# Optimization experiments

Measured on AMD Instinct MI355X. Metric: run time of the kernel, lower is better.

Reference implementation:

```python
import jax, jax.numpy as jnp
import numpy as np

N = 100000
E = 640000
D = 128      # node_dim == edge_dim
H = 256      # conv MLP hidden dim
EPS = 1e-5


def _ln(x, g, b):
    mu = jnp.mean(x, axis=-1, keepdims=True)
    var = jnp.var(x, axis=-1, keepdims=True)
    return (x - mu) * jax.lax.rsqrt(var + EPS) * g + b


def _conv_mlp(x, W1, b1, g1, be1, W2, b2, g2, be2):
    h = _ln(x @ W1 + b1, g1, be1)          # (N, H)
    h = jax.nn.relu(h)
    return _ln(h @ W2 + b2, g2, be2)        # (N, D)


def setup_inputs() -> dict:
    key = jax.random.key(0)
    ks = jax.random.split(key, 6)
    s1 = 1.0 / np.sqrt(D)
    s2 = 1.0 / np.sqrt(H)
    return {
        "x": jax.random.normal(ks[0], (N, D), dtype=jnp.float32),
        "edge_index": jax.random.randint(ks[1], (2, E), 0, N, dtype=jnp.int32),
        "edge_attr": jax.random.normal(ks[2], (E, D), dtype=jnp.float32),
        "W1": jax.random.uniform(ks[3], (D, H), jnp.float32, -s1, s1),
        "b1": jnp.zeros((H,), jnp.float32),
        "g1": jnp.ones((H,), jnp.float32),
        "be1": jnp.zeros((H,), jnp.float32),
        "W2": jax.random.uniform(ks[4], (H, D), jnp.float32, -s2, s2),
        "b2": jnp.zeros((D,), jnp.float32),
        "g2": jnp.ones((D,), jnp.float32),
        "be2": jnp.zeros((D,), jnp.float32),
        "g_out": jnp.ones((D,), jnp.float32),
        "b_out": jnp.zeros((D,), jnp.float32),
    }


def reference(x, edge_index, edge_attr, W1, b1, g1, be1, W2, b2, g2, be2, g_out, b_out):
    # Conv(h[w]) for all nodes once, then gather per edge (vectorized form of
    # the per-node/per-neighbor loops in the torch module).
    conv = _conv_mlp(x, W1, b1, g1, be1, W2, b2, g2, be2)   # (N, D)
    src, dst = edge_index[0], edge_index[1]
    msgs = conv[dst] * edge_attr                            # (E, D): Conv(h[w]) * e[v,w]
    agg = jax.ops.segment_sum(msgs, src, num_segments=N)    # scatter-add into v
    return _ln(agg + x, g_out, b_out)
```

## Files before the change

### kernel.cpp

```cpp
#include <hip/hip_runtime.h>

constexpr int D = 128;
constexpr int H = 256;
constexpr float EPS = 1e-5f;

typedef __attribute__((ext_vector_type(8))) __bf16  bf16x8;
typedef __attribute__((ext_vector_type(4))) float   f32x4;

static __device__ __forceinline__ unsigned short f2bfu(float f) {
    unsigned u = __float_as_uint(f);
    return (unsigned short)((u + 0x7FFFu + ((u >> 16) & 1u)) >> 16);
}
static __device__ __forceinline__ float bf2f(unsigned short u) {
    return __uint_as_float((unsigned)u << 16);
}

static __device__ __forceinline__ f32x4 mfma16x16x32(bf16x8 a, bf16x8 b, f32x4 c) {
    return __builtin_amdgcn_mfma_f32_16x16x32_bf16(a, b, c, 0, 0, 0);
}

static __device__ __forceinline__ void pack_w_elem(
    const float* __restrict__ W, unsigned short* __restrict__ Wp, int K, int Ncols, int e)
{
    int i  = e & 7;
    int l  = (e >> 3) & 63;
    int jt = e >> 9;
    int nt = K >> 5;
    int j  = jt / nt;
    int t  = jt - j * nt;
    int k  = 32 * t + ((l >> 4) << 3) + i;
    int c  = 16 * j + (l & 15);
    Wp[e] = f2bfu(W[(size_t)k * Ncols + c]);
}

__global__ __launch_bounds__(256) void prep_kernel(
    const float* __restrict__ W1, unsigned short* __restrict__ W1p,
    const float* __restrict__ W2, unsigned short* __restrict__ W2p,
    int* __restrict__ counts, int N)
{
    int b = blockIdx.x;
    if (b < 128) {
        pack_w_elem(W1, W1p, D, H, b * 256 + threadIdx.x);
    } else if (b < 256) {
        pack_w_elem(W2, W2p, H, D, (b - 128) * 256 + threadIdx.x);
    } else {
        int i = (b - 256) * 256 + threadIdx.x;
        if (i < N) counts[i] = 0;
    }
}

static __device__ void conv_body(
    unsigned short* __restrict__ Hs,
    const float* __restrict__ x,
    const unsigned short* __restrict__ W1p, const float* __restrict__ b1,
    const float* __restrict__ g1, const float* __restrict__ be1,
    const unsigned short* __restrict__ W2p, const float* __restrict__ b2,
    const float* __restrict__ g2, const float* __restrict__ be2,
    unsigned short* __restrict__ convb, int N, int cblk)
{
    const int wv   = threadIdx.x >> 6;
    const int lane = threadIdx.x & 63;
    const int rrow = lane & 15;
    const int kgrp = lane >> 4;
    const int r0   = cblk * 64 + wv * 16;

    int arow = r0 + rrow; if (arow >= N) arow = N - 1;
    const float* xr = x + (size_t)arow * D + kgrp * 8;
    bf16x8 A1[4];
    #pragma unroll
    for (int t = 0; t < 4; ++t) {
        float4 fa = *(const float4*)(xr + t * 32);
        float4 fb = *(const float4*)(xr + t * 32 + 4);
        bf16x8 a;
        a[0] = (__bf16)fa.x; a[1] = (__bf16)fa.y; a[2] = (__bf16)fa.z; a[3] = (__bf16)fa.w;
        a[4] = (__bf16)fb.x; a[5] = (__bf16)fb.y; a[6] = (__bf16)fb.z; a[7] = (__bf16)fb.w;
        A1[t] = a;
    }

    f32x4 acc[16];
    #pragma unroll
    for (int j = 0; j < 16; ++j) acc[j] = (f32x4){0.f, 0.f, 0.f, 0.f};
    const bf16x8* w1f = (const bf16x8*)W1p;
    #pragma unroll
    for (int j = 0; j < 16; ++j) {
        #pragma unroll
        for (int t = 0; t < 4; ++t) {
            bf16x8 B = w1f[(j * 4 + t) * 64 + lane];
            acc[j] = mfma16x16x32(A1[t], B, acc[j]);
        }
    }

    float b1r[16], g1r[16], be1r[16];
    #pragma unroll
    for (int j = 0; j < 16; ++j) {
        int c = 16 * j + rrow;
        b1r[j] = b1[c]; g1r[j] = g1[c]; be1r[j] = be1[c];
    }

    float s1[4] = {0,0,0,0}, s2[4] = {0,0,0,0};
    #pragma unroll
    for (int j = 0; j < 16; ++j) {
        #pragma unroll
        for (int r = 0; r < 4; ++r) {
            float v = acc[j][r] + b1r[j];
            acc[j][r] = v;
            s1[r] += v; s2[r] += v * v;
        }
    }
    #pragma unroll
    for (int m = 1; m < 16; m <<= 1) {
        #pragma unroll
        for (int r = 0; r < 4; ++r) {
            s1[r] += __shfl_xor(s1[r], m);
            s2[r] += __shfl_xor(s2[r], m);
        }
    }

    #pragma unroll
    for (int r = 0; r < 4; ++r) {
        float mu  = s1[r] * (1.f / H);
        float var = s2[r] * (1.f / H) - mu * mu;
        float rs  = rsqrtf(var + EPS);
        int row = wv * 16 + kgrp * 4 + r;
        #pragma unroll
        for (int j = 0; j < 16; ++j) {
            float h = fmaxf((acc[j][r] - mu) * rs * g1r[j] + be1r[j], 0.f);
            int byte = (row << 9) + ((16 * j + rrow) << 1);
            byte ^= (row & 15) << 4;
            *(unsigned short*)((char*)Hs + byte) = f2bfu(h);
        }
    }

    bf16x8 A2[8];
    #pragma unroll
    for (int t = 0; t < 8; ++t) {
        int row  = wv * 16 + rrow;
        int byte = (row << 9) + ((t * 32 + kgrp * 8) << 1);
        byte ^= (row & 15) << 4;
        A2[t] = *(const bf16x8*)((const char*)Hs + byte);
    }

    f32x4 acc2[8];
    #pragma unroll
    for (int j = 0; j < 8; ++j) acc2[j] = (f32x4){0.f, 0.f, 0.f, 0.f};
    const bf16x8* w2f = (const bf16x8*)W2p;
    #pragma unroll
    for (int j = 0; j < 8; ++j) {
        #pragma unroll
        for (int t = 0; t < 8; ++t) {
            bf16x8 B = w2f[(j * 8 + t) * 64 + lane];
            acc2[j] = mfma16x16x32(A2[t], B, acc2[j]);
        }
    }

    float b2r[8], g2r[8], be2r[8];
    #pragma unroll
    for (int j = 0; j < 8; ++j) {
        int c = 16 * j + rrow;
        b2r[j] = b2[c]; g2r[j] = g2[c]; be2r[j] = be2[c];
    }

    float u1[4] = {0,0,0,0}, u2[4] = {0,0,0,0};
    #pragma unroll
    for (int j = 0; j < 8; ++j) {
        #pragma unroll
        for (int r = 0; r < 4; ++r) {
            float v = acc2[j][r] + b2r[j];
            acc2[j][r] = v;
            u1[r] += v; u2[r] += v * v;
        }
    }
    #pragma unroll
    for (int m = 1; m < 16; m <<= 1) {
        #pragma unroll
        for (int r = 0; r < 4; ++r) {
            u1[r] += __shfl_xor(u1[r], m);
            u2[r] += __shfl_xor(u2[r], m);
        }
    }
    #pragma unroll
    for (int r = 0; r < 4; ++r) {
        float mu  = u1[r] * (1.f / D);
        float var = u2[r] * (1.f / D) - mu * mu;
        float rs  = rsqrtf(var + EPS);
        int grow = r0 + kgrp * 4 + r;
        if (grow < N) {
            #pragma unroll
            for (int j = 0; j < 8; ++j) {
                float o = (acc2[j][r] - mu) * rs * g2r[j] + be2r[j];
                convb[(size_t)grow * D + 16 * j + rrow] = f2bfu(o);
            }
        }
    }
}

__global__ __launch_bounds__(256) void conv_hist_kernel(
    const float* __restrict__ x,
    const unsigned short* __restrict__ W1p, const float* __restrict__ b1,
    const float* __restrict__ g1, const float* __restrict__ be1,
    const unsigned short* __restrict__ W2p, const float* __restrict__ b2,
    const float* __restrict__ g2, const float* __restrict__ be2,
    unsigned short* __restrict__ convb, int N,
    const int* __restrict__ eidx, int* __restrict__ counts, int E, int convBlocks)
{
    __shared__ unsigned short Hs[64 * 256];
    if ((int)blockIdx.x < convBlocks) {
        conv_body(Hs, x, W1p, b1, g1, be1, W2p, b2, g2, be2, convb, N, blockIdx.x);
    } else {
        int e = (blockIdx.x - convBlocks) * 256 + threadIdx.x;
        if (e < E) atomicAdd(&counts[eidx[e]], 1);
    }
}

__global__ __launch_bounds__(256) void scan1_kernel(
    const int* __restrict__ counts, int* __restrict__ row_start,
    int* __restrict__ bsums, int N)
{
    __shared__ int sd[256];
    int t  = threadIdx.x;
    int i0 = blockIdx.x * 1024 + t * 4;
    int c0 = (i0+0 < N) ? counts[i0+0] : 0;
    int c1 = (i0+1 < N) ? counts[i0+1] : 0;
    int c2 = (i0+2 < N) ? counts[i0+2] : 0;
    int c3 = (i0+3 < N) ? counts[i0+3] : 0;
    int s  = c0 + c1 + c2 + c3;
    sd[t] = s;
    __syncthreads();
    #pragma unroll
    for (int off = 1; off < 256; off <<= 1) {
        int v = (t >= off) ? sd[t - off] : 0;
        __syncthreads();
        sd[t] += v;
        __syncthreads();
    }
    int ex = sd[t] - s;
    if (i0+0 < N) row_start[i0+0] = ex;
    if (i0+1 < N) row_start[i0+1] = ex + c0;
    if (i0+2 < N) row_start[i0+2] = ex + c0 + c1;
    if (i0+3 < N) row_start[i0+3] = ex + c0 + c1 + c2;
    if (t == 255) bsums[blockIdx.x] = sd[255];
}

__global__ __launch_bounds__(128) void scan2_kernel(int* __restrict__ bsums, int NB)
{
    __shared__ int sd[128];
    int t = threadIdx.x;
    int v = (t < NB) ? bsums[t] : 0;
    sd[t] = v;
    __syncthreads();
    #pragma unroll
    for (int off = 1; off < 128; off <<= 1) {
        int u = (t >= off) ? sd[t - off] : 0;
        __syncthreads();
        sd[t] += u;
        __syncthreads();
    }
    if (t < NB) bsums[t] = sd[t] - v;
}

__global__ __launch_bounds__(256) void scan3_kernel(
    int* __restrict__ row_start, const int* __restrict__ bsums,
    int* __restrict__ cursor, int N)
{
    int i = blockIdx.x * blockDim.x + threadIdx.x;
    if (i < N) {
        int r = row_start[i] + bsums[i >> 10];
        row_start[i] = r;
        cursor[i]    = r;
    }
}

__global__ __launch_bounds__(256) void fill_kernel(
    const int* __restrict__ eidx, int* __restrict__ cursor,
    int2* __restrict__ edat, int E)
{
    int e = blockIdx.x * blockDim.x + threadIdx.x;
    if (e < E) {
        int s = eidx[e];
        int p = atomicAdd(&cursor[s], 1);
        edat[p] = make_int2(e, eidx[E + e]);
    }
}

__global__ __launch_bounds__(256) void gather_ln_kernel(
    const float* __restrict__ x, const unsigned short* __restrict__ convb,
    const float* __restrict__ eattr,
    const int* __restrict__ row_start, const int2* __restrict__ edat,
    const float* __restrict__ g, const float* __restrict__ b,
    float* __restrict__ out, int N, int E)
{
    int node = blockIdx.x * 4 + (threadIdx.x >> 6);
    if (node >= N) return;
    int lane = threadIdx.x & 63;
    int half = lane >> 5;
    int c4   = (lane & 31) * 4;

    float4 acc = make_float4(0.f, 0.f, 0.f, 0.f);
    int je = (node + 1 < N) ? row_start[node + 1] : E;
    int j  = row_start[node] + half;

    for (; j + 2 < je; j += 4) {
        int2 ea = edat[j];
        int2 eb = edat[j + 2];
        ushort4 ca = *(const ushort4*)(convb + (size_t)ea.y * D + c4);
        float4  aa = *(const float4*) (eattr + (size_t)ea.x * D + c4);
        ushort4 cb = *(const ushort4*)(convb + (size_t)eb.y * D + c4);
        float4  ab = *(const float4*) (eattr + (size_t)eb.x * D + c4);
        acc.x += bf2f(ca.x) * aa.x; acc.y += bf2f(ca.y) * aa.y;
        acc.z += bf2f(ca.z) * aa.z; acc.w += bf2f(ca.w) * aa.w;
        acc.x += bf2f(cb.x) * ab.x; acc.y += bf2f(cb.y) * ab.y;
        acc.z += bf2f(cb.z) * ab.z; acc.w += bf2f(cb.w) * ab.w;
    }
    if (j < je) {
        int2 ea = edat[j];
        ushort4 ca = *(const ushort4*)(convb + (size_t)ea.y * D + c4);
        float4  aa = *(const float4*) (eattr + (size_t)ea.x * D + c4);
        acc.x += bf2f(ca.x) * aa.x; acc.y += bf2f(ca.y) * aa.y;
        acc.z += bf2f(ca.z) * aa.z; acc.w += bf2f(ca.w) * aa.w;
    }

    if (half == 0) {
        float4 xv = *(const float4*)(x + (size_t)node * D + c4);
        acc.x += xv.x; acc.y += xv.y; acc.z += xv.z; acc.w += xv.w;
    }
    acc.x += __shfl_xor(acc.x, 32);
    acc.y += __shfl_xor(acc.y, 32);
    acc.z += __shfl_xor(acc.z, 32);
    acc.w += __shfl_xor(acc.w, 32);

    float s1 = acc.x + acc.y + acc.z + acc.w;
    float s2 = acc.x*acc.x + acc.y*acc.y + acc.z*acc.z + acc.w*acc.w;
    #pragma unroll
    for (int o = 1; o < 32; o <<= 1) {
        s1 += __shfl_xor(s1, o);
        s2 += __shfl_xor(s2, o);
    }
    float mu  = s1 * (1.f / D);
    float var = s2 * (1.f / D) - mu * mu;
    float rs  = rsqrtf(var + EPS);
    if (half == 0) {
        float4 gv = *(const float4*)(g + c4);
        float4 bv = *(const float4*)(b + c4);
        float4 o4;
        o4.x = (acc.x - mu) * rs * gv.x + bv.x;
        o4.y = (acc.y - mu) * rs * gv.y + bv.y;
        o4.z = (acc.z - mu) * rs * gv.z + bv.z;
        o4.w = (acc.w - mu) * rs * gv.w + bv.w;
        *(float4*)(out + (size_t)node * D + c4) = o4;
    }
}

extern "C" void kernel_launch(void* const* d_in, const int* in_sizes, int n_in,
                              void* d_out, int out_size, void* d_ws, size_t ws_size,
                              hipStream_t stream) {
    const float* x     = (const float*)d_in[0];
    const int*   eidx  = (const int*)  d_in[1];
    const float* eattr = (const float*)d_in[2];
    const float* W1    = (const float*)d_in[3];
    const float* b1    = (const float*)d_in[4];
    const float* g1    = (const float*)d_in[5];
    const float* be1   = (const float*)d_in[6];
    const float* W2    = (const float*)d_in[7];
    const float* b2    = (const float*)d_in[8];
    const float* g2    = (const float*)d_in[9];
    const float* be2   = (const float*)d_in[10];
    const float* g_out = (const float*)d_in[11];
    const float* b_out = (const float*)d_in[12];

    const int N = in_sizes[0] / D;
    const int E = in_sizes[1] / 2;

    float* out = (float*)d_out;

    auto align_up = [](size_t v) { return (v + 255) & ~(size_t)255; };
    size_t convB = align_up((size_t)N * D * sizeof(unsigned short));
    size_t cntB  = align_up((size_t)N * sizeof(int));
    size_t rsB   = align_up((size_t)N * sizeof(int));
    size_t bsB   = align_up(128 * sizeof(int));
    size_t edB   = align_up((size_t)E * sizeof(int2));
    size_t w1B   = align_up((size_t)D * H * sizeof(unsigned short));

    char* w = (char*)d_ws;
    unsigned short* convb     = (unsigned short*)(w);
    int*            counts    = (int*)(w + convB);
    int*            row_start = (int*)(w + convB + cntB);
    int*            bsums     = (int*)(w + convB + cntB + rsB);
    int2*           edat      = (int2*)(w + convB + cntB + rsB + bsB);
    unsigned short* W1p       = (unsigned short*)(w + convB + cntB + rsB + bsB + edB);
    unsigned short* W2p       = (unsigned short*)(w + convB + cntB + rsB + bsB + edB + w1B);

    int zeroBlocks = (N + 255) / 256;
    prep_kernel<<<256 + zeroBlocks, 256, 0, stream>>>(W1, W1p, W2, W2p, counts, N);

    int convBlocks = (N + 63) / 64;
    int histBlocks = (E + 255) / 256;
    conv_hist_kernel<<<convBlocks + histBlocks, 256, 0, stream>>>(
        x, W1p, b1, g1, be1, W2p, b2, g2, be2, convb, N, eidx, counts, E, convBlocks);

    int NB = (N + 1023) / 1024;
    scan1_kernel<<<NB, 256, 0, stream>>>(counts, row_start, bsums, N);
    scan2_kernel<<<1, 128, 0, stream>>>(bsums, NB);
    scan3_kernel<<<(N + 255) / 256, 256, 0, stream>>>(row_start, bsums, counts, N);

    fill_kernel<<<(E + 255) / 256, 256, 0, stream>>>(eidx, counts, edat, E);

    gather_ln_kernel<<<(N + 3) / 4, 256, 0, stream>>>(
        x, convb, eattr, row_start, edat, g_out, b_out, out, N, E);
}
```

Baseline: 216.2 us.

## Stage MLP weights through double-buffered LDS instead of per-wave global loads

The conv kernel now loads W1 and W2 cooperatively into a double-buffered shared-memory array in 16 KB chunks, prefetching the next chunk into registers while MFMAs consume the current one. Previously each wave read the packed weights directly from global memory. The aim is to cut redundant global/L2 traffic across the four waves per block and to hide load latency. In exchange LDS per block grows by 32 KB (to 64 KB total), which may lower occupancy, and the extra barriers add synchronisation. The W2 prefetch is also overlapped with the first LayerNorm.

```diff
diff --git a/kernel.cpp b/kernel.cpp
--- a/kernel.cpp
+++ b/kernel.cpp
@@ -49,20 +49,45 @@
     }
 }
 
-static __device__ void conv_body(
-    unsigned short* __restrict__ Hs,
+__global__ __launch_bounds__(256) void conv_hist_kernel(
     const float* __restrict__ x,
     const unsigned short* __restrict__ W1p, const float* __restrict__ b1,
     const float* __restrict__ g1, const float* __restrict__ be1,
     const unsigned short* __restrict__ W2p, const float* __restrict__ b2,
     const float* __restrict__ g2, const float* __restrict__ be2,
-    unsigned short* __restrict__ convb, int N, int cblk)
-{
+    unsigned short* __restrict__ convb, int N,
+    const int* __restrict__ eidx, int* __restrict__ counts, int E, int convBlocks)
+{
+    __shared__ unsigned short Hs[64 * 256];
+    __shared__ unsigned short Ws[2][8192];
+
+    if ((int)blockIdx.x >= convBlocks) {
+        int e = (blockIdx.x - convBlocks) * 256 + threadIdx.x;
+        if (e < E) atomicAdd(&counts[eidx[e]], 1);
+        return;
+    }
+
     const int wv   = threadIdx.x >> 6;
     const int lane = threadIdx.x & 63;
     const int rrow = lane & 15;
     const int kgrp = lane >> 4;
-    const int r0   = cblk * 64 + wv * 16;
+    const int r0   = blockIdx.x * 64 + wv * 16;
+
+    float4 sv0, sv1, sv2, sv3;
+    auto issueW = [&](const unsigned short* Wp, int c) {
+        const float4* s = (const float4*)(Wp + c * 8192);
+        sv0 = s[threadIdx.x];
+        sv1 = s[threadIdx.x + 256];
+        sv2 = s[threadIdx.x + 512];
+        sv3 = s[threadIdx.x + 768];
+    };
+    auto writeS = [&](int b) {
+        float4* d = (float4*)Ws[b];
+        d[threadIdx.x]       = sv0;
+        d[threadIdx.x + 256] = sv1;
+        d[threadIdx.x + 512] = sv2;
+        d[threadIdx.x + 768] = sv3;
+    };
 
     int arow = r0 + rrow; if (arow >= N) arow = N - 1;
     const float* xr = x + (size_t)arow * D + kgrp * 8;
@@ -80,14 +105,22 @@
     f32x4 acc[16];
     #pragma unroll
     for (int j = 0; j < 16; ++j) acc[j] = (f32x4){0.f, 0.f, 0.f, 0.f};
-    const bf16x8* w1f = (const bf16x8*)W1p;
-    #pragma unroll
-    for (int j = 0; j < 16; ++j) {
-        #pragma unroll
-        for (int t = 0; t < 4; ++t) {
-            bf16x8 B = w1f[(j * 4 + t) * 64 + lane];
-            acc[j] = mfma16x16x32(A1[t], B, acc[j]);
-        }
+
+    issueW(W1p, 0); writeS(0); __syncthreads();
+    #pragma unroll
+    for (int c = 0; c < 4; ++c) {
+        if (c < 3) issueW(W1p, c + 1);
+        #pragma unroll
+        for (int jj = 0; jj < 4; ++jj) {
+            #pragma unroll
+            for (int t = 0; t < 4; ++t) {
+                bf16x8 B = *(const bf16x8*)((const char*)Ws[c & 1]
+                             + ((jj * 4 + t) * 512 + lane * 8) * 2);
+                acc[c * 4 + jj] = mfma16x16x32(A1[t], B, acc[c * 4 + jj]);
+            }
+        }
+        if (c < 3) writeS((c + 1) & 1);
+        __syncthreads();
     }
 
     float b1r[16], g1r[16], be1r[16];
@@ -115,6 +148,8 @@
             s2[r] += __shfl_xor(s2[r], m);
         }
     }
+
+    issueW(W2p, 0);
 
     #pragma unroll
     for (int r = 0; r < 4; ++r) {
@@ -140,17 +175,25 @@
         A2[t] = *(const bf16x8*)((const char*)Hs + byte);
     }
 
+    writeS(0); __syncthreads();
+
     f32x4 acc2[8];
     #pragma unroll
     for (int j = 0; j < 8; ++j) acc2[j] = (f32x4){0.f, 0.f, 0.f, 0.f};
-    const bf16x8* w2f = (const bf16x8*)W2p;
-    #pragma unroll
-    for (int j = 0; j < 8; ++j) {
-        #pragma unroll
-        for (int t = 0; t < 8; ++t) {
-            bf16x8 B = w2f[(j * 8 + t) * 64 + lane];
-            acc2[j] = mfma16x16x32(A2[t], B, acc2[j]);
-        }
+    #pragma unroll
+    for (int c = 0; c < 4; ++c) {
+        if (c < 3) issueW(W2p, c + 1);
+        #pragma unroll
+        for (int jj = 0; jj < 2; ++jj) {
+            #pragma unroll
+            for (int t = 0; t < 8; ++t) {
+                bf16x8 B = *(const bf16x8*)((const char*)Ws[c & 1]
+                             + ((jj * 8 + t) * 512 + lane * 8) * 2);
+                acc2[c * 2 + jj] = mfma16x16x32(A2[t], B, acc2[c * 2 + jj]);
+            }
+        }
+        if (c < 3) writeS((c + 1) & 1);
+        __syncthreads();
     }
 
     float b2r[8], g2r[8], be2r[8];
@@ -191,24 +234,6 @@
                 convb[(size_t)grow * D + 16 * j + rrow] = f2bfu(o);
             }
         }
-    }
-}
-
-__global__ __launch_bounds__(256) void conv_hist_kernel(
-    const float* __restrict__ x,
-    const unsigned short* __restrict__ W1p, const float* __restrict__ b1,
-    const float* __restrict__ g1, const float* __restrict__ be1,
-    const unsigned short* __restrict__ W2p, const float* __restrict__ b2,
-    const float* __restrict__ g2, const float* __restrict__ be2,
-    unsigned short* __restrict__ convb, int N,
-    const int* __restrict__ eidx, int* __restrict__ counts, int E, int convBlocks)
-{
-    __shared__ unsigned short Hs[64 * 256];
-    if ((int)blockIdx.x < convBlocks) {
-        conv_body(Hs, x, W1p, b1, g1, be1, W2p, b2, g2, be2, convb, N, blockIdx.x);
-    } else {
-        int e = (blockIdx.x - convBlocks) * 256 + threadIdx.x;
-        if (e < E) atomicAdd(&counts[eidx[e]], 1);
     }
 }
 
```

Result: faster. 211.2 us (-2.3%).
